# Kernel tuning notes

Hardware: AMD Instinct MI355X
Metric: run time of the kernel (lower is better)

The kernel has to match this reference:

```python
import jax, jax.numpy as jnp
import numpy as np

B, T, D = 16, 2048, 1024
NUM_LAYERS = 4
BN_EPS = 1e-5


def setup_inputs() -> dict:
    key = jax.random.key(0)
    ks = jax.random.split(key, 8)
    s = 1.0 / np.sqrt(D)
    x = jax.random.normal(ks[0], (B, T, D), dtype=jnp.float32)
    Wi = jax.random.normal(ks[1], (D, D), dtype=jnp.float32) * s   # SimpleCell input dense kernel
    bi = jnp.zeros((D,), dtype=jnp.float32)                         # SimpleCell input dense bias
    Wh = jax.random.normal(ks[2], (D, D), dtype=jnp.float32) * s   # recurrent dense kernel (no bias)
    mlp_W = jax.random.normal(ks[3], (NUM_LAYERS, D, D), dtype=jnp.float32) * s
    mlp_b = jnp.zeros((NUM_LAYERS, D), dtype=jnp.float32)
    bn_scale = jnp.ones((NUM_LAYERS, D), dtype=jnp.float32)
    bn_bias = jnp.zeros((NUM_LAYERS, D), dtype=jnp.float32)
    return {"x": x, "Wi": Wi, "bi": bi, "Wh": Wh,
            "mlp_W": mlp_W, "mlp_b": mlp_b,
            "bn_scale": bn_scale, "bn_bias": bn_bias}


def reference(x, Wi, bi, Wh, mlp_W, mlp_b, bn_scale, bn_bias):
    # --- linear recurrence (SimpleCell with identity activation) ---
    # h_t = (x_t @ Wi + bi) + h_{t-1} @ Wh,  h_0 = 0
    xp = jnp.einsum('btd,dh->bth', x, Wi) + bi          # pre-project inputs [B,T,H]

    def step(h, xt):
        h = xt + h @ Wh
        return h, h

    h0 = jnp.zeros((x.shape[0], Wh.shape[0]), dtype=x.dtype)
    _, ys = jax.lax.scan(step, h0, jnp.swapaxes(xp, 0, 1))  # scan over time
    y = jnp.swapaxes(ys, 0, 1)                               # [B,T,H]

    # --- residual MLP stack: gelu(BatchNorm(Linear(y))) + y ---
    n_layers = mlp_W.shape[0]
    for l in range(n_layers):
        z = jnp.einsum('bth,hk->btk', y, mlp_W[l]) + mlp_b[l]
        mean = jnp.mean(z, axis=(0, 1))
        var = jnp.var(z, axis=(0, 1))
        zn = (z - mean) * jax.lax.rsqrt(var + BN_EPS) * bn_scale[l] + bn_bias[l]
        y = jax.nn.gelu(zn) + y
    return y
```

## Files before the change

### kernel.cpp

```cpp
#include <hip/hip_runtime.h>
#include <math.h>

#define Bb   16
#define Tt   2048
#define Dd   1024
#define NL   4
#define MTOT (Bb * Tt)

typedef float f32x4 __attribute__((ext_vector_type(4)));
typedef short bf16x8 __attribute__((ext_vector_type(8)));

__device__ __forceinline__ unsigned short f2bf_rne(float x) {
    unsigned u = __float_as_uint(x);
    u += 0x7fffu + ((u >> 16) & 1u);
    return (unsigned short)(u >> 16);
}
__device__ __forceinline__ float bf2f(unsigned short h) {
    return __uint_as_float(((unsigned)h) << 16);
}
__device__ __forceinline__ float gelu_tanh(float x) {
    float x3 = x * x * x;
    float u  = 0.7978845608028654f * (x + 0.044715f * x3);
    return 0.5f * x * (1.0f + tanhf(u));
}
__device__ __forceinline__ void dma16(const void* g, void* l) {
    __builtin_amdgcn_global_load_lds(
        (const __attribute__((address_space(1))) unsigned int*)g,
        (__attribute__((address_space(3))) unsigned int*)l, 16, 0, 0);
}

__global__ __launch_bounds__(256)
void split_bt(const float* __restrict__ B, short* __restrict__ ht,
              short* __restrict__ lt)
{
    __shared__ float tile[32][33];
    const int t  = threadIdx.x;
    const int r  = t >> 3;
    const int c  = (t & 7) * 4;
    const int kb = blockIdx.y * 32;
    const int nb = blockIdx.x * 32;
    float4 v = *reinterpret_cast<const float4*>(
        &B[(size_t)(kb + r) * Dd + nb + c]);
    tile[r][c + 0] = v.x; tile[r][c + 1] = v.y;
    tile[r][c + 2] = v.z; tile[r][c + 3] = v.w;
    __syncthreads();
    unsigned h[4], lo[4];
#pragma unroll
    for (int q = 0; q < 4; ++q) {
        float f = tile[c + q][r];
        unsigned short hh = f2bf_rne(f);
        float rem = f - bf2f(hh);
        h[q]  = hh;
        lo[q] = f2bf_rne(rem);
    }
    uint2 hw, lw;
    hw.x = h[0]  | (h[1]  << 16); hw.y = h[2]  | (h[3]  << 16);
    lw.x = lo[0] | (lo[1] << 16); lw.y = lo[2] | (lo[3] << 16);
    const int n = nb + r;
    const int s = (c >> 3) ^ ((n >> 1) & 3);
    size_t off = ((size_t)(blockIdx.y * 1024 + n) * 4 + s) * 8 + (c & 4);
    *reinterpret_cast<uint2*>(&ht[off]) = hw;
    *reinterpret_cast<uint2*>(&lt[off]) = lw;
}

template<int MODE, int NT, int S3, int WSPLIT>
__device__ __forceinline__ void gemm_body(
    short* lds, int bx, int by,
    const float* __restrict__ Af,
    const short* __restrict__ Bth, const short* __restrict__ Btl,
    const float* __restrict__ bias,
    const float* __restrict__ Sin,
    float* __restrict__ Cf,
    short* __restrict__ Woh, short* __restrict__ Wol,
    int m, int tstart)
{
    constexpr int NJ    = NT / 32;
    constexpr int APL   = 5120;
    constexpr int BBASE = (S3 ? 2 : 1) * APL;
    constexpr int BPL   = NT * 32;

    const int tid  = threadIdx.x;
    const int lane = tid & 63;
    const int w    = tid >> 6;
    const int n0   = bx * NT;
    const int m0g  = (MODE == 2) ? (by * Tt + tstart) : (by * 128);
    const int wm0  = (w >> 1) * 64;
    const int wn0  = (w & 1) * (NT / 2);
    const int ln   = lane & 15;
    const int ar   = tid >> 3;
    const int ac   = (tid & 7) * 4;

    int  arow_src[4]; bool avalid[4];
#pragma unroll
    for (int p = 0; p < 4; ++p) {
        int rg = m0g + p * 32 + ar;
        bool v = true;
        if (MODE == 1) v = ((rg & (Tt - 1)) >= m);
        avalid[p]   = v;
        arow_src[p] = (MODE >= 1 && v) ? (rg - m) : rg;
    }

    f32x4 acc[4][NJ];
#pragma unroll
    for (int i = 0; i < 4; ++i)
#pragma unroll
        for (int j = 0; j < NJ; ++j) acc[i][j] = (f32x4){0.f, 0.f, 0.f, 0.f};

    int a_off[4];
#pragma unroll
    for (int i = 0; i < 4; ++i)
        a_off[i] = (wm0 + i * 16 + ln) * 40 + (lane >> 4) * 8;
    const int nlb    = wn0 + ln;
    const int b_off0 = BBASE + nlb * 32 +
                       (((lane >> 4) ^ ((nlb >> 1) & 3)) << 3);

    for (int kt = 0; kt < 32; ++kt) {
        __syncthreads();
#pragma unroll
        for (int p = 0; p < 4; ++p) {
            float4 v = *reinterpret_cast<const float4*>(
                &Af[(size_t)arow_src[p] * Dd + kt * 32 + ac]);
            if (MODE == 1 && !avalid[p]) v = make_float4(0.f, 0.f, 0.f, 0.f);
            int wo = (p * 32 + ar) * 40 + ac;
            unsigned short h0 = f2bf_rne(v.x), h1 = f2bf_rne(v.y),
                           h2 = f2bf_rne(v.z), h3 = f2bf_rne(v.w);
            uint2 hw;
            hw.x = (unsigned)h0 | ((unsigned)h1 << 16);
            hw.y = (unsigned)h2 | ((unsigned)h3 << 16);
            *reinterpret_cast<uint2*>(&lds[wo]) = hw;
            if (S3) {
                unsigned short g0 = f2bf_rne(v.x - bf2f(h0)),
                               g1 = f2bf_rne(v.y - bf2f(h1)),
                               g2 = f2bf_rne(v.z - bf2f(h2)),
                               g3 = f2bf_rne(v.w - bf2f(h3));
                uint2 lw;
                lw.x = (unsigned)g0 | ((unsigned)g1 << 16);
                lw.y = (unsigned)g2 | ((unsigned)g3 << 16);
                *reinterpret_cast<uint2*>(&lds[wo + APL]) = lw;
            }
        }
#pragma unroll
        for (int q = 0; q < NT / 64; ++q) {
            size_t gfo = ((size_t)(kt * 1024 + n0 + q * 64 + (tid >> 2))
                          * 4 + (tid & 3)) * 8;
            dma16(&Bth[gfo], &lds[BBASE + q * 2048 + w * 512]);
            if (S3)
                dma16(&Btl[gfo], &lds[BBASE + BPL + q * 2048 + w * 512]);
        }
        __syncthreads();
        bf16x8 ah[4], al[4];
#pragma unroll
        for (int i = 0; i < 4; ++i) {
            ah[i] = *reinterpret_cast<const bf16x8*>(&lds[a_off[i]]);
            if (S3)
                al[i] = *reinterpret_cast<const bf16x8*>(&lds[a_off[i] + APL]);
        }
#pragma unroll
        for (int j = 0; j < NJ; ++j) {
            const bf16x8 bh = *reinterpret_cast<const bf16x8*>(
                &lds[b_off0 + j * 512]);
#pragma unroll
            for (int i = 0; i < 4; ++i)
                acc[i][j] = __builtin_amdgcn_mfma_f32_16x16x32_bf16(
                    ah[i], bh, acc[i][j], 0, 0, 0);
            if (S3) {
                const bf16x8 bl = *reinterpret_cast<const bf16x8*>(
                    &lds[b_off0 + j * 512 + BPL]);
#pragma unroll
                for (int i = 0; i < 4; ++i) {
                    acc[i][j] = __builtin_amdgcn_mfma_f32_16x16x32_bf16(
                        ah[i], bl, acc[i][j], 0, 0, 0);
                    acc[i][j] = __builtin_amdgcn_mfma_f32_16x16x32_bf16(
                        al[i], bh, acc[i][j], 0, 0, 0);
                }
            }
        }
    }

#pragma unroll
    for (int j = 0; j < NJ; ++j) {
        int cl  = wn0 + j * 16 + ln;
        int col = n0 + cl;
        float bj = (MODE == 0 && bias) ? bias[col] : 0.f;
#pragma unroll
        for (int i = 0; i < 4; ++i) {
            int rbase = m0g + wm0 + i * 16 + (lane >> 4) * 4;
            float vv[4];
#pragma unroll
            for (int e = 0; e < 4; ++e) {
                size_t off = (size_t)(rbase + e) * Dd + col;
                float v = acc[i][j][e] + bj;
                if (MODE >= 1) v += Sin[off];
                Cf[off] = v;
                vv[e] = v;
            }
            if (WSPLIT) {
                unsigned short h0 = f2bf_rne(vv[0]), h1 = f2bf_rne(vv[1]),
                               h2 = f2bf_rne(vv[2]), h3 = f2bf_rne(vv[3]);
                unsigned short l0 = f2bf_rne(vv[0] - bf2f(h0)),
                               l1 = f2bf_rne(vv[1] - bf2f(h1)),
                               l2 = f2bf_rne(vv[2] - bf2f(h2)),
                               l3 = f2bf_rne(vv[3] - bf2f(h3));
                uint2 hw, lw;
                hw.x = (unsigned)h0 | ((unsigned)h1 << 16);
                hw.y = (unsigned)h2 | ((unsigned)h3 << 16);
                lw.x = (unsigned)l0 | ((unsigned)l1 << 16);
                lw.y = (unsigned)l2 | ((unsigned)l3 << 16);
                int kt2 = rbase >> 5;
                int sl  = (rbase >> 3) & 3;
                int e0  = rbase & 7;
                size_t so = ((size_t)(kt2 * 1024 + col) * 4 +
                             (sl ^ ((col >> 1) & 3))) * 8 + e0;
                *reinterpret_cast<uint2*>(&Woh[so]) = hw;
                *reinterpret_cast<uint2*>(&Wol[so]) = lw;
            }
        }
    }
}

template<int MODE, int NT, int S3>
__global__ __launch_bounds__(256, 2)
void mfma_gemm(const float* __restrict__ Af,
               const short* __restrict__ Bth, const short* __restrict__ Btl,
               const float* __restrict__ bias,
               const float* __restrict__ Sin,
               float* __restrict__ Cf,
               int m, int tstart)
{
    constexpr int LSZ = (S3 ? 2 : 1) * (5120 + NT * 32);
    __shared__ __align__(16) short lds[LSZ];
    gemm_body<MODE, NT, S3, 0>(lds, blockIdx.x, blockIdx.y,
                               Af, Bth, Btl, bias, Sin, Cf,
                               nullptr, nullptr, m, tstart);
}

__global__ __launch_bounds__(256, 2)
void fused_ls(const float* __restrict__ Sfrom, float* __restrict__ Sto,
              const float* __restrict__ Pfrom, float* __restrict__ Pto,
              const short* __restrict__ Bqh, const short* __restrict__ Bql,
              short* __restrict__ Bqoh, short* __restrict__ Bqol,
              int m)
{
    __shared__ __align__(16) short lds[2 * (5120 + 8192)];
    if (blockIdx.y < 16) {
        int sq  = blockIdx.y;
        int sbx = blockIdx.x + ((sq & 1) << 2);
        int sby = sq >> 1;
        gemm_body<0, 128, 1, 1>(lds, sbx, sby, Pfrom, Bqh, Bql,
                                nullptr, nullptr, Pto, Bqoh, Bqol, 0, 0);
    } else {
        gemm_body<1, 256, 1, 0>(lds, blockIdx.x, blockIdx.y - 16,
                                Sfrom, Bqh, Bql, nullptr, Sfrom, Sto,
                                nullptr, nullptr, m, 0);
    }
}

__global__ __launch_bounds__(512, 2)
void mlp_gemm(const float* __restrict__ Af,
              const short* __restrict__ Bth,
              const float* __restrict__ bias,
              float* __restrict__ Cf,
              float* __restrict__ psum, float* __restrict__ psq)
{
    constexpr int APL = 5120;
    constexpr int BB  = APL;
    __shared__ __align__(16) short lds[APL + 8192];

    const int tid  = threadIdx.x;
    const int lane = tid & 63;
    const int w    = tid >> 6;
    const int n0   = blockIdx.x * 256;
    const int m0g  = blockIdx.y * 128;
    const int wm0  = (w >> 2) * 64;
    const int wn0  = (w & 3) * 64;
    const int ln   = lane & 15;
    const int ar   = tid >> 2;
    const int ac   = (tid & 3) * 8;

    f32x4 acc[4][4];
#pragma unroll
    for (int i = 0; i < 4; ++i)
#pragma unroll
        for (int j = 0; j < 4; ++j) acc[i][j] = (f32x4){0.f, 0.f, 0.f, 0.f};

    int a_off[4];
#pragma unroll
    for (int i = 0; i < 4; ++i)
        a_off[i] = (wm0 + i * 16 + ln) * 40 + (lane >> 4) * 8;
    const int nlb    = wn0 + ln;
    const int b_off0 = BB + nlb * 32 +
                       (((lane >> 4) ^ ((nlb >> 1) & 3)) << 3);

    for (int kt = 0; kt < 32; ++kt) {
        __syncthreads();
        {
            const float* p = &Af[(size_t)(m0g + ar) * Dd + kt * 32 + ac];
            float4 v0 = *reinterpret_cast<const float4*>(p);
            float4 v1 = *reinterpret_cast<const float4*>(p + 4);
            unsigned short h0 = f2bf_rne(v0.x), h1 = f2bf_rne(v0.y),
                           h2 = f2bf_rne(v0.z), h3 = f2bf_rne(v0.w),
                           h4 = f2bf_rne(v1.x), h5 = f2bf_rne(v1.y),
                           h6 = f2bf_rne(v1.z), h7 = f2bf_rne(v1.w);
            int4 hw;
            hw.x = (int)((unsigned)h0 | ((unsigned)h1 << 16));
            hw.y = (int)((unsigned)h2 | ((unsigned)h3 << 16));
            hw.z = (int)((unsigned)h4 | ((unsigned)h5 << 16));
            hw.w = (int)((unsigned)h6 | ((unsigned)h7 << 16));
            *reinterpret_cast<int4*>(&lds[ar * 40 + ac]) = hw;
        }
#pragma unroll
        for (int q = 0; q < 2; ++q) {
            size_t gfo = ((size_t)(kt * 1024 + n0 + q * 128 + (tid >> 2))
                          * 4 + (tid & 3)) * 8;
            dma16(&Bth[gfo], &lds[BB + q * 4096 + w * 512]);
        }
        __syncthreads();
        bf16x8 ah[4];
#pragma unroll
        for (int i = 0; i < 4; ++i)
            ah[i] = *reinterpret_cast<const bf16x8*>(&lds[a_off[i]]);
#pragma unroll
        for (int j = 0; j < 4; ++j) {
            const bf16x8 bh = *reinterpret_cast<const bf16x8*>(
                &lds[b_off0 + j * 512]);
#pragma unroll
            for (int i = 0; i < 4; ++i)
                acc[i][j] = __builtin_amdgcn_mfma_f32_16x16x32_bf16(
                    ah[i], bh, acc[i][j], 0, 0, 0);
        }
    }

    float* bnF = reinterpret_cast<float*>(lds);
    __syncthreads();
    if (tid < 256) { bnF[tid] = 0.f; bnF[256 + tid] = 0.f; }
    __syncthreads();
#pragma unroll
    for (int j = 0; j < 4; ++j) {
        int cl  = wn0 + j * 16 + ln;
        int col = n0 + cl;
        float bj = bias[col];
        float sv = 0.f, sq = 0.f;
#pragma unroll
        for (int i = 0; i < 4; ++i) {
            int rbase = m0g + wm0 + i * 16 + (lane >> 4) * 4;
#pragma unroll
            for (int e = 0; e < 4; ++e) {
                size_t off = (size_t)(rbase + e) * Dd + col;
                float v = acc[i][j][e] + bj;
                Cf[off] = v;
                sv += v; sq += v * v;
            }
        }
        atomicAdd(&bnF[cl], sv); atomicAdd(&bnF[256 + cl], sq);
    }
    __syncthreads();
    if (tid < 256) {
        psum[(size_t)blockIdx.y * Dd + n0 + tid] = bnF[tid];
        psq [(size_t)blockIdx.y * Dd + n0 + tid] = bnF[256 + tid];
    }
}

__global__ __launch_bounds__(256)
void bn_stats(const float* __restrict__ ps, const float* __restrict__ pq,
              const float* __restrict__ scale, const float* __restrict__ bias,
              float* __restrict__ Av, float* __restrict__ Cv)
{
    const int d = blockIdx.x * 256 + threadIdx.x;
    float s = 0.f, q = 0.f;
    for (int p = 0; p < 256; ++p) {
        s += ps[p * Dd + d];
        q += pq[p * Dd + d];
    }
    const float invN = 1.0f / 32768.0f;
    float mean = s * invN;
    float var  = q * invN - mean * mean;
    float rs   = rsqrtf(var + 1e-5f);
    float a    = rs * scale[d];
    Av[d] = a;
    Cv[d] = bias[d] - mean * a;
}

__global__ __launch_bounds__(256)
void residual_gelu(const float* __restrict__ Z, const float* __restrict__ Yin,
                   float* __restrict__ Yout,
                   const float* __restrict__ Av, const float* __restrict__ Cv)
{
    const float4* z4 = reinterpret_cast<const float4*>(Z);
    const float4* y4 = reinterpret_cast<const float4*>(Yin);
    float4*       o4 = reinterpret_cast<float4*>(Yout);
    const float4* a4 = reinterpret_cast<const float4*>(Av);
    const float4* c4 = reinterpret_cast<const float4*>(Cv);
    const int n4 = MTOT * Dd / 4;
    for (int i = blockIdx.x * blockDim.x + threadIdx.x; i < n4;
         i += gridDim.x * blockDim.x) {
        int d4 = i & (Dd / 4 - 1);
        float4 z = z4[i], y = y4[i], a = a4[d4], c = c4[d4];
        float4 o;
        o.x = gelu_tanh(fmaf(z.x, a.x, c.x)) + y.x;
        o.y = gelu_tanh(fmaf(z.y, a.y, c.y)) + y.y;
        o.z = gelu_tanh(fmaf(z.z, a.z, c.z)) + y.z;
        o.w = gelu_tanh(fmaf(z.w, a.w, c.w)) + y.w;
        o4[i] = o;
    }
}

extern "C" void kernel_launch(void* const* d_in, const int* in_sizes, int n_in,
                              void* d_out, int out_size, void* d_ws, size_t ws_size,
                              hipStream_t stream)
{
    const float* x    = (const float*)d_in[0];
    const float* Wi   = (const float*)d_in[1];
    const float* bi   = (const float*)d_in[2];
    const float* Wh   = (const float*)d_in[3];
    const float* mlpW = (const float*)d_in[4];
    const float* mlpb = (const float*)d_in[5];
    const float* bns  = (const float*)d_in[6];
    const float* bnb  = (const float*)d_in[7];
    float* out = (float*)d_out;

    const size_t NE = (size_t)MTOT * Dd;
    const size_t MM = (size_t)Dd * Dd;
    float* ws   = (float*)d_ws;
    float* S0   = ws;
    float* Pa   = S0 + NE;
    float* Pb   = Pa + MM;
    float* psum = Pb + MM;
    float* psq  = psum + 256 * Dd;
    float* abuf = psq + 256 * Dd;
    float* cbuf = abuf + Dd;
    short* Bq0h = (short*)(cbuf + Dd);
    short* Bq0l = Bq0h + MM;
    short* Bq1h = Bq0l + MM;
    short* Bq1l = Bq1h + MM;
    short* BmH[NL]; short* BmL[NL];
    {
        short* p = Bq1l + MM;
        for (int l = 0; l < NL; ++l) { BmH[l] = p; p += MM; BmL[l] = p; p += MM; }
    }

    const dim3 gBig(4, 256);
    const dim3 gF  (4, 272);
    const dim3 gSeq(8, 16);
    const dim3 gBt (32, 32);

    split_bt<<<gBt, 256, 0, stream>>>(Wi, Bq0h, Bq0l);
    split_bt<<<gBt, 256, 0, stream>>>(Wh, Bq1h, Bq1l);
    for (int l = 0; l < NL; ++l)
        split_bt<<<gBt, 256, 0, stream>>>(mlpW + (size_t)l * MM, BmH[l], BmL[l]);

    mfma_gemm<0, 256, 1><<<gBig, 256, 0, stream>>>(
        x, Bq0h, Bq0l, bi, nullptr, S0, 0, 0);

    fused_ls<<<gF, 256, 0, stream>>>(S0, out, Wh, Pa, Bq1h, Bq1l, Bq0h, Bq0l, 1);
    fused_ls<<<gF, 256, 0, stream>>>(out, S0, Pa, Pb, Bq0h, Bq0l, Bq1h, Bq1l, 2);
    fused_ls<<<gF, 256, 0, stream>>>(S0, out, Pb, Pa, Bq1h, Bq1l, Bq0h, Bq0l, 4);
    fused_ls<<<gF, 256, 0, stream>>>(out, S0, Pa, Pb, Bq0h, Bq0l, Bq1h, Bq1l, 8);
    fused_ls<<<gF, 256, 0, stream>>>(S0, out, Pb, Pa, Bq1h, Bq1l, Bq0h, Bq0l, 16);
    fused_ls<<<gF, 256, 0, stream>>>(out, S0, Pa, Pb, Bq0h, Bq0l, Bq1h, Bq1l, 32);
    fused_ls<<<gF, 256, 0, stream>>>(S0, out, Pb, Pa, Bq1h, Bq1l, Bq0h, Bq0l, 64);

    for (int i = 1; i < 16; ++i)
        mfma_gemm<2, 128, 1><<<gSeq, 256, 0, stream>>>(
            out, Bq0h, Bq0l, nullptr, out, out, 128, 128 * i);

    for (int l = 0; l < NL; ++l) {
        mlp_gemm<<<gBig, 512, 0, stream>>>(
            out, BmH[l], mlpb + (size_t)l * Dd, S0, psum, psq);
        bn_stats<<<4, 256, 0, stream>>>(psum, psq, bns + (size_t)l * Dd,
                                        bnb + (size_t)l * Dd, abuf, cbuf);
        residual_gelu<<<2048, 256, 0, stream>>>(S0, out, out, abuf, cbuf);
    }
}
```

Baseline: 3.750 ms.

## Use 512-thread 128x256 tiles for input and log-step recurrence GEMMs

Replaces the 256-thread GEMM body with a 512-thread, 8-wave version that computes 128x256 tiles. The power-squaring branch of fused_ls now uses the same wide tile instead of 128-column tiles, which shrinks the grid from 272 to 264 rows of blocks and increases B-tile reuse per A load. The chunk-carry GEMM moves into a dedicated kernel that adds its result into the output in place. The aim is fewer A reloads and conversions per output element; the cost is higher register and LDS pressure per block, which may lower occupancy.

```diff
diff --git a/kernel.cpp b/kernel.cpp
--- a/kernel.cpp
+++ b/kernel.cpp
@@ -63,8 +63,8 @@
     *reinterpret_cast<uint2*>(&lt[off]) = lw;
 }
 
-template<int MODE, int NT, int S3, int WSPLIT>
-__device__ __forceinline__ void gemm_body(
+template<int MODE, int WSPLIT>
+__device__ __forceinline__ void gemm512_body(
     short* lds, int bx, int by,
     const float* __restrict__ Af,
     const short* __restrict__ Bth, const short* __restrict__ Btl,
@@ -72,113 +72,103 @@
     const float* __restrict__ Sin,
     float* __restrict__ Cf,
     short* __restrict__ Woh, short* __restrict__ Wol,
-    int m, int tstart)
-{
-    constexpr int NJ    = NT / 32;
-    constexpr int APL   = 5120;
-    constexpr int BBASE = (S3 ? 2 : 1) * APL;
-    constexpr int BPL   = NT * 32;
+    int m)
+{
+    constexpr int APL = 5120;
+    constexpr int BB  = 2 * APL;
+    constexpr int BPL = 8192;
 
     const int tid  = threadIdx.x;
     const int lane = tid & 63;
     const int w    = tid >> 6;
-    const int n0   = bx * NT;
-    const int m0g  = (MODE == 2) ? (by * Tt + tstart) : (by * 128);
-    const int wm0  = (w >> 1) * 64;
-    const int wn0  = (w & 1) * (NT / 2);
+    const int n0   = bx * 256;
+    const int m0g  = by * 128;
+    const int wm0  = (w >> 2) * 64;
+    const int wn0  = (w & 3) * 64;
     const int ln   = lane & 15;
-    const int ar   = tid >> 3;
-    const int ac   = (tid & 7) * 4;
-
-    int  arow_src[4]; bool avalid[4];
-#pragma unroll
-    for (int p = 0; p < 4; ++p) {
-        int rg = m0g + p * 32 + ar;
-        bool v = true;
-        if (MODE == 1) v = ((rg & (Tt - 1)) >= m);
-        avalid[p]   = v;
-        arow_src[p] = (MODE >= 1 && v) ? (rg - m) : rg;
-    }
-
-    f32x4 acc[4][NJ];
+    const int ar   = tid >> 2;
+    const int ac   = (tid & 3) * 8;
+
+    const int rg = m0g + ar;
+    bool avalid = true;
+    if (MODE == 1) avalid = ((rg & (Tt - 1)) >= m);
+    const size_t arow = (size_t)((MODE == 1 && avalid) ? (rg - m) : rg);
+
+    f32x4 acc[4][4];
 #pragma unroll
     for (int i = 0; i < 4; ++i)
 #pragma unroll
-        for (int j = 0; j < NJ; ++j) acc[i][j] = (f32x4){0.f, 0.f, 0.f, 0.f};
+        for (int j = 0; j < 4; ++j) acc[i][j] = (f32x4){0.f, 0.f, 0.f, 0.f};
 
     int a_off[4];
 #pragma unroll
     for (int i = 0; i < 4; ++i)
         a_off[i] = (wm0 + i * 16 + ln) * 40 + (lane >> 4) * 8;
     const int nlb    = wn0 + ln;
-    const int b_off0 = BBASE + nlb * 32 +
+    const int b_off0 = BB + nlb * 32 +
                        (((lane >> 4) ^ ((nlb >> 1) & 3)) << 3);
 
     for (int kt = 0; kt < 32; ++kt) {
         __syncthreads();
-#pragma unroll
-        for (int p = 0; p < 4; ++p) {
-            float4 v = *reinterpret_cast<const float4*>(
-                &Af[(size_t)arow_src[p] * Dd + kt * 32 + ac]);
-            if (MODE == 1 && !avalid[p]) v = make_float4(0.f, 0.f, 0.f, 0.f);
-            int wo = (p * 32 + ar) * 40 + ac;
-            unsigned short h0 = f2bf_rne(v.x), h1 = f2bf_rne(v.y),
-                           h2 = f2bf_rne(v.z), h3 = f2bf_rne(v.w);
-            uint2 hw;
-            hw.x = (unsigned)h0 | ((unsigned)h1 << 16);
-            hw.y = (unsigned)h2 | ((unsigned)h3 << 16);
-            *reinterpret_cast<uint2*>(&lds[wo]) = hw;
-            if (S3) {
-                unsigned short g0 = f2bf_rne(v.x - bf2f(h0)),
-                               g1 = f2bf_rne(v.y - bf2f(h1)),
-                               g2 = f2bf_rne(v.z - bf2f(h2)),
-                               g3 = f2bf_rne(v.w - bf2f(h3));
-                uint2 lw;
-                lw.x = (unsigned)g0 | ((unsigned)g1 << 16);
-                lw.y = (unsigned)g2 | ((unsigned)g3 << 16);
-                *reinterpret_cast<uint2*>(&lds[wo + APL]) = lw;
-            }
-        }
-#pragma unroll
-        for (int q = 0; q < NT / 64; ++q) {
-            size_t gfo = ((size_t)(kt * 1024 + n0 + q * 64 + (tid >> 2))
-                          * 4 + (tid & 3)) * 8;
-            dma16(&Bth[gfo], &lds[BBASE + q * 2048 + w * 512]);
-            if (S3)
-                dma16(&Btl[gfo], &lds[BBASE + BPL + q * 2048 + w * 512]);
+        {
+            const float* p = &Af[arow * Dd + kt * 32 + ac];
+            float4 v0 = *reinterpret_cast<const float4*>(p);
+            float4 v1 = *reinterpret_cast<const float4*>(p + 4);
+            float f[8] = {v0.x, v0.y, v0.z, v0.w, v1.x, v1.y, v1.z, v1.w};
+            if (MODE == 1 && !avalid) {
+#pragma unroll
+                for (int e = 0; e < 8; ++e) f[e] = 0.f;
+            }
+            unsigned hh[8], ll[8];
+#pragma unroll
+            for (int e = 0; e < 8; ++e) {
+                unsigned short h = f2bf_rne(f[e]);
+                hh[e] = h;
+                ll[e] = f2bf_rne(f[e] - bf2f(h));
+            }
+            int4 hw, lw;
+            hw.x = (int)(hh[0] | (hh[1] << 16)); hw.y = (int)(hh[2] | (hh[3] << 16));
+            hw.z = (int)(hh[4] | (hh[5] << 16)); hw.w = (int)(hh[6] | (hh[7] << 16));
+            lw.x = (int)(ll[0] | (ll[1] << 16)); lw.y = (int)(ll[2] | (ll[3] << 16));
+            lw.z = (int)(ll[4] | (ll[5] << 16)); lw.w = (int)(ll[6] | (ll[7] << 16));
+            *reinterpret_cast<int4*>(&lds[ar * 40 + ac])       = hw;
+            *reinterpret_cast<int4*>(&lds[ar * 40 + ac + APL]) = lw;
+        }
+#pragma unroll
+        for (int q = 0; q < 2; ++q) {
+            int f = q * 512 + tid;
+            size_t gfo = ((size_t)(kt * 1024 + n0 + (f >> 2)) * 4 + (f & 3)) * 8;
+            short* dh = &lds[BB + q * 4096 + w * 512];
+            dma16(&Bth[gfo], dh);
+            dma16(&Btl[gfo], dh + BPL);
         }
         __syncthreads();
         bf16x8 ah[4], al[4];
 #pragma unroll
         for (int i = 0; i < 4; ++i) {
             ah[i] = *reinterpret_cast<const bf16x8*>(&lds[a_off[i]]);
-            if (S3)
-                al[i] = *reinterpret_cast<const bf16x8*>(&lds[a_off[i] + APL]);
-        }
-#pragma unroll
-        for (int j = 0; j < NJ; ++j) {
+            al[i] = *reinterpret_cast<const bf16x8*>(&lds[a_off[i] + APL]);
+        }
+#pragma unroll
+        for (int j = 0; j < 4; ++j) {
             const bf16x8 bh = *reinterpret_cast<const bf16x8*>(
                 &lds[b_off0 + j * 512]);
-#pragma unroll
-            for (int i = 0; i < 4; ++i)
+            const bf16x8 bl = *reinterpret_cast<const bf16x8*>(
+                &lds[b_off0 + j * 512 + BPL]);
+#pragma unroll
+            for (int i = 0; i < 4; ++i) {
                 acc[i][j] = __builtin_amdgcn_mfma_f32_16x16x32_bf16(
                     ah[i], bh, acc[i][j], 0, 0, 0);
-            if (S3) {
-                const bf16x8 bl = *reinterpret_cast<const bf16x8*>(
-                    &lds[b_off0 + j * 512 + BPL]);
-#pragma unroll
-                for (int i = 0; i < 4; ++i) {
-                    acc[i][j] = __builtin_amdgcn_mfma_f32_16x16x32_bf16(
-                        ah[i], bl, acc[i][j], 0, 0, 0);
-                    acc[i][j] = __builtin_amdgcn_mfma_f32_16x16x32_bf16(
-                        al[i], bh, acc[i][j], 0, 0, 0);
-                }
-            }
-        }
-    }
-
-#pragma unroll
-    for (int j = 0; j < NJ; ++j) {
+                acc[i][j] = __builtin_amdgcn_mfma_f32_16x16x32_bf16(
+                    ah[i], bl, acc[i][j], 0, 0, 0);
+                acc[i][j] = __builtin_amdgcn_mfma_f32_16x16x32_bf16(
+                    al[i], bh, acc[i][j], 0, 0, 0);
+            }
+        }
+    }
+
+#pragma unroll
+    for (int j = 0; j < 4; ++j) {
         int cl  = wn0 + j * 16 + ln;
         int col = n0 + cl;
         float bj = (MODE == 0 && bias) ? bias[col] : 0.f;
@@ -190,7 +180,7 @@
             for (int e = 0; e < 4; ++e) {
                 size_t off = (size_t)(rbase + e) * Dd + col;
                 float v = acc[i][j][e] + bj;
-                if (MODE >= 1) v += Sin[off];
+                if (MODE == 1) v += Sin[off];
                 Cf[off] = v;
                 vv[e] = v;
             }
@@ -218,40 +208,142 @@
     }
 }
 
-template<int MODE, int NT, int S3>
-__global__ __launch_bounds__(256, 2)
-void mfma_gemm(const float* __restrict__ Af,
-               const short* __restrict__ Bth, const short* __restrict__ Btl,
-               const float* __restrict__ bias,
-               const float* __restrict__ Sin,
-               float* __restrict__ Cf,
-               int m, int tstart)
-{
-    constexpr int LSZ = (S3 ? 2 : 1) * (5120 + NT * 32);
-    __shared__ __align__(16) short lds[LSZ];
-    gemm_body<MODE, NT, S3, 0>(lds, blockIdx.x, blockIdx.y,
-                               Af, Bth, Btl, bias, Sin, Cf,
-                               nullptr, nullptr, m, tstart);
-}
-
-__global__ __launch_bounds__(256, 2)
+template<int MODE>
+__global__ __launch_bounds__(512, 2)
+void mfma_gemm512(const float* __restrict__ Af,
+                  const short* __restrict__ Bth, const short* __restrict__ Btl,
+                  const float* __restrict__ bias,
+                  const float* __restrict__ Sin,
+                  float* __restrict__ Cf, int m)
+{
+    __shared__ __align__(16) short lds[2 * 5120 + 2 * 8192];
+    gemm512_body<MODE, 0>(lds, blockIdx.x, blockIdx.y,
+                          Af, Bth, Btl, bias, Sin, Cf, nullptr, nullptr, m);
+}
+
+__global__ __launch_bounds__(512, 2)
 void fused_ls(const float* __restrict__ Sfrom, float* __restrict__ Sto,
               const float* __restrict__ Pfrom, float* __restrict__ Pto,
               const short* __restrict__ Bqh, const short* __restrict__ Bql,
               short* __restrict__ Bqoh, short* __restrict__ Bqol,
               int m)
 {
-    __shared__ __align__(16) short lds[2 * (5120 + 8192)];
-    if (blockIdx.y < 16) {
-        int sq  = blockIdx.y;
-        int sbx = blockIdx.x + ((sq & 1) << 2);
-        int sby = sq >> 1;
-        gemm_body<0, 128, 1, 1>(lds, sbx, sby, Pfrom, Bqh, Bql,
-                                nullptr, nullptr, Pto, Bqoh, Bqol, 0, 0);
+    __shared__ __align__(16) short lds[2 * 5120 + 2 * 8192];
+    if (blockIdx.y < 8) {
+        gemm512_body<0, 1>(lds, blockIdx.x, blockIdx.y, Pfrom, Bqh, Bql,
+                           nullptr, nullptr, Pto, Bqoh, Bqol, 0);
     } else {
-        gemm_body<1, 256, 1, 0>(lds, blockIdx.x, blockIdx.y - 16,
-                                Sfrom, Bqh, Bql, nullptr, Sfrom, Sto,
-                                nullptr, nullptr, m, 0);
+        gemm512_body<1, 0>(lds, blockIdx.x, blockIdx.y - 8,
+                           Sfrom, Bqh, Bql, nullptr, Sfrom, Sto,
+                           nullptr, nullptr, m);
+    }
+}
+
+__global__ __launch_bounds__(256, 2)
+void carry_gemm(const float* __restrict__ Af,
+                const short* __restrict__ Bth, const short* __restrict__ Btl,
+                float* __restrict__ Cf, int tstart)
+{
+    constexpr int APL   = 5120;
+    constexpr int BBASE = 2 * APL;
+    constexpr int BPL   = 4096;
+    __shared__ __align__(16) short lds[BBASE + 2 * BPL];
+
+    const int tid  = threadIdx.x;
+    const int lane = tid & 63;
+    const int w    = tid >> 6;
+    const int n0   = blockIdx.x * 128;
+    const int m0g  = blockIdx.y * Tt + tstart;
+    const int wm0  = (w >> 1) * 64;
+    const int wn0  = (w & 1) * 64;
+    const int ln   = lane & 15;
+    const int ar   = tid >> 3;
+    const int ac   = (tid & 7) * 4;
+
+    int arow_src[4];
+#pragma unroll
+    for (int p = 0; p < 4; ++p)
+        arow_src[p] = m0g + p * 32 + ar - 128;
+
+    f32x4 acc[4][4];
+#pragma unroll
+    for (int i = 0; i < 4; ++i)
+#pragma unroll
+        for (int j = 0; j < 4; ++j) acc[i][j] = (f32x4){0.f, 0.f, 0.f, 0.f};
+
+    int a_off[4];
+#pragma unroll
+    for (int i = 0; i < 4; ++i)
+        a_off[i] = (wm0 + i * 16 + ln) * 40 + (lane >> 4) * 8;
+    const int nlb    = wn0 + ln;
+    const int b_off0 = BBASE + nlb * 32 +
+                       (((lane >> 4) ^ ((nlb >> 1) & 3)) << 3);
+
+    for (int kt = 0; kt < 32; ++kt) {
+        __syncthreads();
+#pragma unroll
+        for (int p = 0; p < 4; ++p) {
+            float4 v = *reinterpret_cast<const float4*>(
+                &Af[(size_t)arow_src[p] * Dd + kt * 32 + ac]);
+            int wo = (p * 32 + ar) * 40 + ac;
+            unsigned short h0 = f2bf_rne(v.x), h1 = f2bf_rne(v.y),
+                           h2 = f2bf_rne(v.z), h3 = f2bf_rne(v.w);
+            unsigned short g0 = f2bf_rne(v.x - bf2f(h0)),
+                           g1 = f2bf_rne(v.y - bf2f(h1)),
+                           g2 = f2bf_rne(v.z - bf2f(h2)),
+                           g3 = f2bf_rne(v.w - bf2f(h3));
+            uint2 hw, lw;
+            hw.x = (unsigned)h0 | ((unsigned)h1 << 16);
+            hw.y = (unsigned)h2 | ((unsigned)h3 << 16);
+            lw.x = (unsigned)g0 | ((unsigned)g1 << 16);
+            lw.y = (unsigned)g2 | ((unsigned)g3 << 16);
+            *reinterpret_cast<uint2*>(&lds[wo])       = hw;
+            *reinterpret_cast<uint2*>(&lds[wo + APL]) = lw;
+        }
+#pragma unroll
+        for (int q = 0; q < 2; ++q) {
+            size_t gfo = ((size_t)(kt * 1024 + n0 + q * 64 + (tid >> 2))
+                          * 4 + (tid & 3)) * 8;
+            dma16(&Bth[gfo], &lds[BBASE + q * 2048 + w * 512]);
+            dma16(&Btl[gfo], &lds[BBASE + BPL + q * 2048 + w * 512]);
+        }
+        __syncthreads();
+        bf16x8 ah[4], al[4];
+#pragma unroll
+        for (int i = 0; i < 4; ++i) {
+            ah[i] = *reinterpret_cast<const bf16x8*>(&lds[a_off[i]]);
+            al[i] = *reinterpret_cast<const bf16x8*>(&lds[a_off[i] + APL]);
+        }
+#pragma unroll
+        for (int j = 0; j < 4; ++j) {
+            const bf16x8 bh = *reinterpret_cast<const bf16x8*>(
+                &lds[b_off0 + j * 512]);
+            const bf16x8 bl = *reinterpret_cast<const bf16x8*>(
+                &lds[b_off0 + j * 512 + BPL]);
+#pragma unroll
+            for (int i = 0; i < 4; ++i) {
+                acc[i][j] = __builtin_amdgcn_mfma_f32_16x16x32_bf16(
+                    ah[i], bh, acc[i][j], 0, 0, 0);
+                acc[i][j] = __builtin_amdgcn_mfma_f32_16x16x32_bf16(
+                    ah[i], bl, acc[i][j], 0, 0, 0);
+                acc[i][j] = __builtin_amdgcn_mfma_f32_16x16x32_bf16(
+                    al[i], bh, acc[i][j], 0, 0, 0);
+            }
+        }
+    }
+
+#pragma unroll
+    for (int j = 0; j < 4; ++j) {
+        int col = n0 + wn0 + j * 16 + ln;
+#pragma unroll
+        for (int i = 0; i < 4; ++i) {
+            int rbase = m0g + wm0 + i * 16 + (lane >> 4) * 4;
+#pragma unroll
+            for (int e = 0; e < 4; ++e) {
+                size_t off = (size_t)(rbase + e) * Dd + col;
+                Cf[off] += acc[i][j][e];
+            }
+        }
     }
 }
 
@@ -439,7 +531,7 @@
     }
 
     const dim3 gBig(4, 256);
-    const dim3 gF  (4, 272);
+    const dim3 gF  (4, 264);
     const dim3 gSeq(8, 16);
     const dim3 gBt (32, 32);
 
@@ -448,20 +540,19 @@
     for (int l = 0; l < NL; ++l)
         split_bt<<<gBt, 256, 0, stream>>>(mlpW + (size_t)l * MM, BmH[l], BmL[l]);
 
-    mfma_gemm<0, 256, 1><<<gBig, 256, 0, stream>>>(
-        x, Bq0h, Bq0l, bi, nullptr, S0, 0, 0);
-
-    fused_ls<<<gF, 256, 0, stream>>>(S0, out, Wh, Pa, Bq1h, Bq1l, Bq0h, Bq0l, 1);
-    fused_ls<<<gF, 256, 0, stream>>>(out, S0, Pa, Pb, Bq0h, Bq0l, Bq1h, Bq1l, 2);
-    fused_ls<<<gF, 256, 0, stream>>>(S0, out, Pb, Pa, Bq1h, Bq1l, Bq0h, Bq0l, 4);
-    fused_ls<<<gF, 256, 0, stream>>>(out, S0, Pa, Pb, Bq0h, Bq0l, Bq1h, Bq1l, 8);
-    fused_ls<<<gF, 256, 0, stream>>>(S0, out, Pb, Pa, Bq1h, Bq1l, Bq0h, Bq0l, 16);
-    fused_ls<<<gF, 256, 0, stream>>>(out, S0, Pa, Pb, Bq0h, Bq0l, Bq1h, Bq1l, 32);
-    fused_ls<<<gF, 256, 0, stream>>>(S0, out, Pb, Pa, Bq1h, Bq1l, Bq0h, Bq0l, 64);
+    mfma_gemm512<0><<<gBig, 512, 0, stream>>>(
+        x, Bq0h, Bq0l, bi, nullptr, S0, 0);
+
+    fused_ls<<<gF, 512, 0, stream>>>(S0, out, Wh, Pa, Bq1h, Bq1l, Bq0h, Bq0l, 1);
+    fused_ls<<<gF, 512, 0, stream>>>(out, S0, Pa, Pb, Bq0h, Bq0l, Bq1h, Bq1l, 2);
+    fused_ls<<<gF, 512, 0, stream>>>(S0, out, Pb, Pa, Bq1h, Bq1l, Bq0h, Bq0l, 4);
+    fused_ls<<<gF, 512, 0, stream>>>(out, S0, Pa, Pb, Bq0h, Bq0l, Bq1h, Bq1l, 8);
+    fused_ls<<<gF, 512, 0, stream>>>(S0, out, Pb, Pa, Bq1h, Bq1l, Bq0h, Bq0l, 16);
+    fused_ls<<<gF, 512, 0, stream>>>(out, S0, Pa, Pb, Bq0h, Bq0l, Bq1h, Bq1l, 32);
+    fused_ls<<<gF, 512, 0, stream>>>(S0, out, Pb, Pa, Bq1h, Bq1l, Bq0h, Bq0l, 64);
 
     for (int i = 1; i < 16; ++i)
-        mfma_gemm<2, 128, 1><<<gSeq, 256, 0, stream>>>(
-            out, Bq0h, Bq0l, nullptr, out, out, 128, 128 * i);
+        carry_gemm<<<gSeq, 256, 0, stream>>>(out, Bq0h, Bq0l, out, 128 * i);
 
     for (int l = 0; l < NL; ++l) {
         mlp_gemm<<<gBig, 512, 0, stream>>>(
```

New measurement: 4.499 ms. 20.0% more time.
